# Optimization experiments

Hardware: AMD Instinct MI355X
Metric: run time of the kernel (lower is better)

The kernel has to match this reference:

```python
import jax, jax.numpy as jnp
import numpy as np

N = 100000  # num nodes


def gcn_conv(x, edge_index, W, b):
    # PyG GCNConv (eval): x' = D^-1/2 (A + I) D^-1/2 (x @ W) + b
    x = x @ W  # [N, out]
    row = jnp.concatenate([edge_index[0], jnp.arange(N)])  # sources (+ self loops)
    col = jnp.concatenate([edge_index[1], jnp.arange(N)])  # targets (+ self loops)
    ones = jnp.ones(row.shape[0], dtype=x.dtype)
    deg = jax.ops.segment_sum(ones, col, num_segments=N)
    dis = jnp.where(deg > 0, jax.lax.rsqrt(jnp.maximum(deg, 1.0)), 0.0)
    norm = dis[row] * dis[col]  # [E+N]
    msg = norm[:, None] * x[row]  # gather + scale
    out = jax.ops.segment_sum(msg, col, num_segments=N)  # scatter-add
    return out + b


def setup_inputs() -> dict:
    key = jax.random.key(0)
    k1, k2, k3, k4 = jax.random.split(key, 4)
    F_in, H, F_out = 512, 16, 40
    x = jax.random.normal(k1, (N, F_in), dtype=jnp.float32)
    edge_index = jax.random.randint(k2, (2, 3200000), 0, N, dtype=jnp.int64)
    W1 = jax.random.normal(k3, (F_in, H), dtype=jnp.float32) / np.sqrt(F_in)
    b1 = jnp.zeros((H,), dtype=jnp.float32)
    W2 = jax.random.normal(k4, (H, F_out), dtype=jnp.float32) / np.sqrt(H)
    b2 = jnp.zeros((F_out,), dtype=jnp.float32)
    return {"x": x, "edge_index": edge_index, "W1": W1, "b1": b1, "W2": W2, "b2": b2}


def reference(x, edge_index, W1, b1, W2, b2):
    # eval mode: no drop_edge, no dropout
    h = jax.nn.relu(gcn_conv(x, edge_index, W1, b1))
    return gcn_conv(h, edge_index, W2, b2)
```

## Files before the change

kernel.cpp:

```cpp
#include <hip/hip_runtime.h>

#define F_IN 512
#define HDIM 16
#define F_OUT 40
#define BTGT 64
#define REPL 8
#define NCH 512

typedef unsigned short ushortT;

__device__ __forceinline__ unsigned f2bf(float f) {
  unsigned u = __float_as_uint(f);
  u += 0x7FFF + ((u >> 16) & 1);
  return u >> 16;
}
__device__ __forceinline__ float bf2f(ushortT b) {
  return __uint_as_float(((unsigned)b) << 16);
}

__device__ __forceinline__ int load_src(const void* ei, int is64, int e) {
  return is64 ? (int)((const unsigned int*)ei)[2 * (long long)e] : ((const int*)ei)[e];
}
__device__ __forceinline__ int load_dst(const void* ei, int is64, int e, int E) {
  long long i = (long long)E + e;
  return is64 ? (int)((const unsigned int*)ei)[2 * i] : ((const int*)ei)[i];
}

extern "C" __global__ void k_init(int* __restrict__ hist, int m, int* __restrict__ flag) {
  int i = blockIdx.x * blockDim.x + threadIdx.x;
  if (i < m) hist[i] = 0;
  if (i == 0) *flag = 1;
}

extern "C" __global__ void k_detect(const unsigned int* __restrict__ w, int npairs,
                                    int* __restrict__ flag) {
  int i = blockIdx.x * blockDim.x + threadIdx.x;
  if (i < npairs && w[2 * i + 1] != 0u) atomicAnd(flag, 0);
}

extern "C" __global__ __launch_bounds__(256) void k_hist(const void* __restrict__ ei, int E,
                                                         int echunk, int* __restrict__ hist,
                                                         int NBK,
                                                         const int* __restrict__ flag) {
  extern __shared__ int lh[];
  int g = blockIdx.x, t = threadIdx.x;
  for (int i = t; i < NBK; i += 256) lh[i] = 0;
  __syncthreads();
  int is64 = *flag;
  int e0 = g * echunk;
  int e1 = e0 + echunk;
  if (e1 > E) e1 = E;
  if (e0 < e1) {
    if (is64 && ((E & 1) == 0)) {
      const int* w32 = (const int*)ei;
      int evend = e0 + ((e1 - e0) & ~1);
      for (int e = e0 + 2 * t; e + 1 < evend + 2; e += 512) {
        if (e + 1 >= e1) break;
        int4 d4 = *(const int4*)(w32 + 2 * ((size_t)E + e));
        atomicAdd(&lh[(unsigned)d4.x >> 6], 1);
        atomicAdd(&lh[(unsigned)d4.z >> 6], 1);
      }
      for (int e = evend + t; e < e1; e += 256)
        atomicAdd(&lh[(unsigned)load_dst(ei, 1, e, E) >> 6], 1);
    } else {
      for (int e = e0 + t; e < e1; e += 256)
        atomicAdd(&lh[(unsigned)load_dst(ei, is64, e, E) >> 6], 1);
    }
  }
  __syncthreads();
  int repl = g & (REPL - 1);
  for (int i = t; i < NBK; i += 256) {
    int v = lh[i];
    if (v) atomicAdd(&hist[i * REPL + repl], v);
  }
}

extern "C" __global__ __launch_bounds__(1024) void k_scanb(const int* __restrict__ hist,
                                                           int* __restrict__ boffs,
                                                           int* __restrict__ bcur, int M) {
  __shared__ int sh[1024];
  int tid = threadIdx.x;
  int C = (M + 1023) / 1024;
  int base = tid * C;
  int s = 0;
  for (int k = 0; k < C; k++) {
    int idx = base + k;
    if (idx < M) s += hist[idx];
  }
  sh[tid] = s;
  __syncthreads();
  for (int d = 1; d < 1024; d <<= 1) {
    int t2 = (tid >= d) ? sh[tid - d] : 0;
    __syncthreads();
    sh[tid] += t2;
    __syncthreads();
  }
  int run = sh[tid] - s;
  for (int k = 0; k < C; k++) {
    int idx = base + k;
    if (idx < M) {
      int v = hist[idx];
      boffs[idx] = run;
      bcur[idx] = run;
      run += v;
    }
  }
  if (tid == 1023) boffs[M] = run;
}

extern "C" __global__ __launch_bounds__(256) void k_bucket(const void* __restrict__ ei, int E,
                                                           int echunk, int* __restrict__ bcur,
                                                           unsigned int* __restrict__ bked,
                                                           const int* __restrict__ flag) {
  int g = blockIdx.x, t = threadIdx.x;
  int is64 = *flag;
  int repl = g & (REPL - 1);
  int e0 = g * echunk;
  int e1 = e0 + echunk;
  if (e1 > E) e1 = E;
  if (e0 >= e1) return;
  if (is64 && ((E & 1) == 0)) {
    const int* w32 = (const int*)ei;
    int evend = e0 + ((e1 - e0) & ~1);
    for (int e = e0 + 2 * t; e + 1 < evend + 2; e += 512) {
      if (e + 1 >= e1) break;
      int4 s4 = *(const int4*)(w32 + 2 * (size_t)e);
      int4 d4 = *(const int4*)(w32 + 2 * ((size_t)E + e));
      {
        int idx = ((unsigned)d4.x >> 6) * REPL + repl;
        int p = atomicAdd(&bcur[idx], 1);
        __builtin_nontemporal_store(
            (unsigned)s4.x | ((unsigned)(d4.x & (BTGT - 1)) << 20), &bked[p]);
      }
      {
        int idx = ((unsigned)d4.z >> 6) * REPL + repl;
        int p = atomicAdd(&bcur[idx], 1);
        __builtin_nontemporal_store(
            (unsigned)s4.z | ((unsigned)(d4.z & (BTGT - 1)) << 20), &bked[p]);
      }
    }
    for (int e = evend + t; e < e1; e += 256) {
      int r = load_src(ei, 1, e);
      int c = load_dst(ei, 1, e, E);
      int idx = ((unsigned)c >> 6) * REPL + repl;
      int p = atomicAdd(&bcur[idx], 1);
      __builtin_nontemporal_store(
          (unsigned)r | ((unsigned)(c & (BTGT - 1)) << 20), &bked[p]);
    }
  } else {
    for (int e = e0 + t; e < e1; e += 256) {
      int r = load_src(ei, is64, e);
      int c = load_dst(ei, is64, e, E);
      int idx = ((unsigned)c >> 6) * REPL + repl;
      int p = atomicAdd(&bcur[idx], 1);
      __builtin_nontemporal_store(
          (unsigned)r | ((unsigned)(c & (BTGT - 1)) << 20), &bked[p]);
    }
  }
}

extern "C" __global__ __launch_bounds__(256) void k_degb(const unsigned int* __restrict__ bked,
                                                         const int* __restrict__ boffs,
                                                         float* __restrict__ dis, int n) {
  __shared__ int lc[BTGT];
  int b = blockIdx.x, t = threadIdx.x;
  if (t < BTGT) lc[t] = 0;
  __syncthreads();
  int beg = boffs[b * REPL], end = boffs[(b + 1) * REPL];
  for (int p = beg + t; p < end; p += 256)
    atomicAdd(&lc[__builtin_nontemporal_load(&bked[p]) >> 20], 1);
  __syncthreads();
  if (t < BTGT) {
    int i = b * BTGT + t;
    if (i < n) dis[i] = rsqrtf((float)lc[t] + 1.0f);
  }
}

extern "C" __global__ __launch_bounds__(256) void k_mm1s(
    const float* __restrict__ x, const float* __restrict__ W1, const float* __restrict__ dis,
    ushortT* __restrict__ hs, int n) {
  __shared__ float xs[256 * 32];
  __shared__ float w1s[F_IN * HDIM];
  int t = threadIdx.x;
  int row0 = blockIdx.x * 256;
  {
    const float4* wg = (const float4*)W1;
    float4* wl = (float4*)w1s;
    for (int i = t; i < F_IN * HDIM / 4; i += 256) wl[i] = wg[i];
  }
  int r = row0 + t;
  bool active = (r < n);
  bool fullblk = (row0 + 255 < n);
  float acc[HDIM];
#pragma unroll
  for (int j = 0; j < HDIM; j++) acc[j] = 0.f;

  float4* xs4 = (float4*)xs;
  for (int kc = 0; kc < F_IN / 32; kc++) {
    __syncthreads();
    if (fullblk) {
#pragma unroll
      for (int it = 0; it < 8; it++) {
        int f = it * 256 + t;
        int r2 = f >> 3, fi = f & 7;
        float4 v = ((const float4*)(x + (size_t)(row0 + r2) * F_IN + kc * 32))[fi];
        xs4[r2 * 8 + (fi ^ (r2 & 7))] = v;
      }
    } else {
      for (int it = 0; it < 8; it++) {
        int f = it * 256 + t;
        int r2 = f >> 3, fi = f & 7;
        float4 v = make_float4(0.f, 0.f, 0.f, 0.f);
        if (row0 + r2 < n)
          v = ((const float4*)(x + (size_t)(row0 + r2) * F_IN + kc * 32))[fi];
        xs4[r2 * 8 + (fi ^ (r2 & 7))] = v;
      }
    }
    __syncthreads();
    if (active) {
#pragma unroll
      for (int i = 0; i < 8; i++) {
        int ii = i ^ (t & 7);
        float4 xv = xs4[t * 8 + ii];
        float xk[4] = {xv.x, xv.y, xv.z, xv.w};
        int kb = kc * 32 + i * 4;
#pragma unroll
        for (int kk = 0; kk < 4; kk++) {
          const float4* wr = (const float4*)(w1s + (size_t)(kb + kk) * HDIM);
#pragma unroll
          for (int q = 0; q < HDIM / 4; q++) {
            float4 wv = wr[q];
            acc[4 * q + 0] = fmaf(xk[kk], wv.x, acc[4 * q + 0]);
            acc[4 * q + 1] = fmaf(xk[kk], wv.y, acc[4 * q + 1]);
            acc[4 * q + 2] = fmaf(xk[kk], wv.z, acc[4 * q + 2]);
            acc[4 * q + 3] = fmaf(xk[kk], wv.w, acc[4 * q + 3]);
          }
        }
      }
    }
  }
  if (active) {
    float d = dis[r];
    unsigned wds[8];
#pragma unroll
    for (int q = 0; q < 8; q++) {
      unsigned lo = f2bf(d * acc[2 * q]);
      unsigned hi = f2bf(d * acc[2 * q + 1]);
      wds[q] = lo | (hi << 16);
    }
    uint4* o = (uint4*)(hs + (size_t)r * HDIM);
    o[0] = make_uint4(wds[0], wds[1], wds[2], wds[3]);
    o[1] = make_uint4(wds[4], wds[5], wds[6], wds[7]);
  }
}

extern "C" __global__ __launch_bounds__(256) void k_agg1(
    const ushortT* __restrict__ hs, const unsigned int* __restrict__ bked,
    const int* __restrict__ boffs, const float* __restrict__ dis,
    const float* __restrict__ b1, ushortT* __restrict__ zs, int n) {
  __shared__ float acc[BTGT * HDIM];
  int b = blockIdx.x, t = threadIdx.x;
  int g = t >> 4, j = t & 15;
  for (int k = t; k < BTGT * HDIM; k += 256) acc[k] = 0.f;
  __syncthreads();
  int beg = boffs[b * REPL], end = boffs[(b + 1) * REPL];
  int total = end - beg;
  int nfull = total >> 7;
  int pbase = beg + (g << 3);
  for (int s2 = 0; s2 < nfull; s2++) {
    int p = pbase + (s2 << 7);
    unsigned u[8];
    float v[8];
#pragma unroll
    for (int k = 0; k < 8; k++) u[k] = __builtin_nontemporal_load(&bked[p + k]);
#pragma unroll
    for (int k = 0; k < 8; k++) v[k] = bf2f(hs[(size_t)(u[k] & 0xFFFFFu) * HDIM + j]);
#pragma unroll
    for (int k = 0; k < 8; k++) atomicAdd(&acc[(u[k] >> 20) * HDIM + j], v[k]);
  }
  for (int p = beg + (nfull << 7) + g; p < end; p += 16) {
    unsigned u = __builtin_nontemporal_load(&bked[p]);
    float v = bf2f(hs[(size_t)(u & 0xFFFFFu) * HDIM + j]);
    atomicAdd(&acc[(u >> 20) * HDIM + j], v);
  }
  __syncthreads();
  for (int il = g; il < BTGT; il += 16) {
    int i = b * BTGT + il;
    if (i < n) {
      float di = dis[i];
      float v = di * (acc[il * HDIM + j] + bf2f(hs[(size_t)i * HDIM + j])) + b1[j];
      v = fmaxf(v, 0.f);
      zs[(size_t)i * HDIM + j] = (ushortT)f2bf(di * v);
    }
  }
}

extern "C" __global__ __launch_bounds__(256) void k_agg2f(
    const ushortT* __restrict__ zs, const unsigned int* __restrict__ bked,
    const int* __restrict__ boffs, const float* __restrict__ dis,
    const float* __restrict__ W2, const float* __restrict__ b2, float* __restrict__ out,
    int n) {
  __shared__ float acc[BTGT * HDIM];
  __shared__ float w2s[HDIM * F_OUT];
  __shared__ float b2s[F_OUT];
  int b = blockIdx.x, t = threadIdx.x;
  int g = t >> 4, j = t & 15;
  for (int k = t; k < BTGT * HDIM; k += 256) acc[k] = 0.f;
  for (int k = t; k < HDIM * F_OUT; k += 256) w2s[k] = W2[k];
  if (t < F_OUT) b2s[t] = b2[t];
  __syncthreads();
  int beg = boffs[b * REPL], end = boffs[(b + 1) * REPL];
  int total = end - beg;
  int nfull = total >> 7;
  int pbase = beg + (g << 3);
  for (int s2 = 0; s2 < nfull; s2++) {
    int p = pbase + (s2 << 7);
    unsigned u[8];
    float v[8];
#pragma unroll
    for (int k = 0; k < 8; k++) u[k] = __builtin_nontemporal_load(&bked[p + k]);
#pragma unroll
    for (int k = 0; k < 8; k++) v[k] = bf2f(zs[(size_t)(u[k] & 0xFFFFFu) * HDIM + j]);
#pragma unroll
    for (int k = 0; k < 8; k++) atomicAdd(&acc[(u[k] >> 20) * HDIM + j], v[k]);
  }
  for (int p = beg + (nfull << 7) + g; p < end; p += 16) {
    unsigned u = __builtin_nontemporal_load(&bked[p]);
    float v = bf2f(zs[(size_t)(u & 0xFFFFFu) * HDIM + j]);
    atomicAdd(&acc[(u >> 20) * HDIM + j], v);
  }
  __syncthreads();
  for (int il = g; il < BTGT; il += 16) {
    int i = b * BTGT + il;
    if (i < n) {
      float di = dis[i];
      acc[il * HDIM + j] = di * (acc[il * HDIM + j] + bf2f(zs[(size_t)i * HDIM + j]));
    }
  }
  __syncthreads();
  int il = t >> 2, qo = t & 3;
  int i = b * BTGT + il;
  if (i < n) {
    float tv[HDIM];
#pragma unroll
    for (int k = 0; k < HDIM; k++) tv[k] = acc[il * HDIM + k];
#pragma unroll
    for (int jj = 0; jj < 10; jj++) {
      int col = qo * 10 + jj;
      float s = b2s[col];
#pragma unroll
      for (int k = 0; k < HDIM; k++) s = fmaf(tv[k], w2s[k * F_OUT + col], s);
      out[(size_t)i * F_OUT + col] = s;
    }
  }
}

extern "C" void kernel_launch(void* const* d_in, const int* in_sizes, int n_in,
                              void* d_out, int out_size, void* d_ws, size_t ws_size,
                              hipStream_t stream) {
  const float* x = (const float*)d_in[0];
  const void* ei = d_in[1];
  const float* W1 = (const float*)d_in[2];
  const float* b1 = (const float*)d_in[3];
  const float* W2 = (const float*)d_in[4];
  const float* b2 = (const float*)d_in[5];
  float* out = (float*)d_out;

  const int n = in_sizes[0] / F_IN;
  const int E = in_sizes[1] / 2;
  const int NBK = (n + BTGT - 1) / BTGT;
  const int M = NBK * REPL;
  int echunk = (E + NCH - 1) / NCH;
  echunk = (echunk + 1) & ~1;

  char* w = (char*)d_ws;
  auto alloc = [&](size_t bytes) {
    char* p = w;
    w += (bytes + 255) & ~(size_t)255;
    return p;
  };
  int* flag = (int*)alloc(4);
  int* hist = (int*)alloc((size_t)M * 4);
  int* boffs = (int*)alloc((size_t)(M + 1) * 4);
  int* bcur = (int*)alloc((size_t)M * 4);
  float* dis = (float*)alloc((size_t)n * 4);
  unsigned int* bked = (unsigned int*)alloc((size_t)E * 4);
  ushortT* hs = (ushortT*)alloc((size_t)n * HDIM * 2);
  ushortT* zs = (ushortT*)alloc((size_t)n * HDIM * 2);

  dim3 B(256);
  hipLaunchKernelGGL(k_init, dim3((M + 255) / 256), B, 0, stream, hist, M, flag);
  int npairs = 4096;
  if (npairs > E) npairs = E;
  hipLaunchKernelGGL(k_detect, dim3((npairs + 255) / 256), B, 0, stream,
                     (const unsigned int*)ei, npairs, flag);
  hipLaunchKernelGGL(k_hist, dim3(NCH), B, (size_t)NBK * 4, stream, ei, E, echunk, hist, NBK,
                     flag);
  hipLaunchKernelGGL(k_scanb, dim3(1), dim3(1024), 0, stream, hist, boffs, bcur, M);
  hipLaunchKernelGGL(k_bucket, dim3(NCH), B, 0, stream, ei, E, echunk, bcur, bked, flag);
  hipLaunchKernelGGL(k_degb, dim3(NBK), B, 0, stream, bked, boffs, dis, n);
  hipLaunchKernelGGL(k_mm1s, dim3((n + 255) / 256), B, 0, stream, x, W1, dis, hs, n);
  hipLaunchKernelGGL(k_agg1, dim3(NBK), B, 0, stream, hs, bked, boffs, dis, b1, zs, n);
  hipLaunchKernelGGL(k_agg2f, dim3(NBK), B, 0, stream, zs, bked, boffs, dis, W2, b2, out, n);
}
```

Baseline: 962.7 us.

## Stage bucketed edges through LDS and gather two bf16 features per thread

In the degree and both aggregation kernels, each block now copies its bucketed edge list into shared memory in coalesced chunks of 2048 before processing it, replacing per-thread strided nontemporal global loads. The aggregation gather now reads a 32-bit word holding two bf16 features per thread, so 8 threads cover a 16-wide row and twice as many edges are in flight per block. Launch bounds request 2 blocks per CU. The cost is extra LDS use and two barriers per chunk, and the atomic count per thread doubles.

```diff
diff --git a/kernel.cpp b/kernel.cpp
--- a/kernel.cpp
+++ b/kernel.cpp
@@ -6,6 +6,7 @@
 #define BTGT 64
 #define REPL 8
 #define NCH 512
+#define ECH 2048
 
 typedef unsigned short ushortT;
 
@@ -16,6 +17,12 @@
 }
 __device__ __forceinline__ float bf2f(ushortT b) {
   return __uint_as_float(((unsigned)b) << 16);
+}
+__device__ __forceinline__ float bf2f_lo(unsigned w) {
+  return __uint_as_float(w << 16);
+}
+__device__ __forceinline__ float bf2f_hi(unsigned w) {
+  return __uint_as_float(w & 0xFFFF0000u);
 }
 
 __device__ __forceinline__ int load_src(const void* ei, int is64, int e) {
@@ -159,17 +166,23 @@
   }
 }
 
-extern "C" __global__ __launch_bounds__(256) void k_degb(const unsigned int* __restrict__ bked,
-                                                         const int* __restrict__ boffs,
-                                                         float* __restrict__ dis, int n) {
+extern "C" __global__ __launch_bounds__(256, 2) void k_degb(
+    const unsigned int* __restrict__ bked, const int* __restrict__ boffs,
+    float* __restrict__ dis, int n) {
   __shared__ int lc[BTGT];
+  __shared__ unsigned ebd[ECH];
   int b = blockIdx.x, t = threadIdx.x;
   if (t < BTGT) lc[t] = 0;
   __syncthreads();
   int beg = boffs[b * REPL], end = boffs[(b + 1) * REPL];
-  for (int p = beg + t; p < end; p += 256)
-    atomicAdd(&lc[__builtin_nontemporal_load(&bked[p]) >> 20], 1);
-  __syncthreads();
+  for (int cbeg = beg; cbeg < end; cbeg += ECH) {
+    int len = end - cbeg;
+    if (len > ECH) len = ECH;
+    for (int i = t; i < len; i += 256) ebd[i] = bked[cbeg + i];
+    __syncthreads();
+    for (int i = t; i < len; i += 256) atomicAdd(&lc[ebd[i] >> 20], 1);
+    __syncthreads();
+  }
   if (t < BTGT) {
     int i = b * BTGT + t;
     if (i < n) dis[i] = rsqrtf((float)lc[t] + 1.0f);
@@ -254,36 +267,56 @@
   }
 }
 
-extern "C" __global__ __launch_bounds__(256) void k_agg1(
+__device__ __forceinline__ void agg_body(const ushortT* __restrict__ feat,
+                                         const unsigned int* __restrict__ bked,
+                                         unsigned* __restrict__ eb,
+                                         float* __restrict__ acc, int beg, int end, int t) {
+  int g = t >> 3, j2 = t & 7;
+  for (int cbeg = beg; cbeg < end; cbeg += ECH) {
+    int len = end - cbeg;
+    if (len > ECH) len = ECH;
+    for (int i = t; i < len; i += 256) eb[i] = bked[cbeg + i];
+    __syncthreads();
+    int nf = len >> 8;
+    for (int s = 0; s < nf; s++) {
+      int base = (s << 8) + (g << 3);
+      unsigned u[8];
+#pragma unroll
+      for (int k = 0; k < 8; k++) u[k] = eb[base + k];
+      unsigned w[8];
+#pragma unroll
+      for (int k = 0; k < 8; k++)
+        w[k] = *(const unsigned*)(feat + ((size_t)(u[k] & 0xFFFFFu) << 4) + (j2 << 1));
+#pragma unroll
+      for (int k = 0; k < 8; k++) {
+        int a = ((u[k] >> 20) << 4) + (j2 << 1);
+        atomicAdd(&acc[a], bf2f_lo(w[k]));
+        atomicAdd(&acc[a + 1], bf2f_hi(w[k]));
+      }
+    }
+    for (int i = (nf << 8) + g; i < len; i += 32) {
+      unsigned u = eb[i];
+      unsigned w = *(const unsigned*)(feat + ((size_t)(u & 0xFFFFFu) << 4) + (j2 << 1));
+      int a = ((u >> 20) << 4) + (j2 << 1);
+      atomicAdd(&acc[a], bf2f_lo(w));
+      atomicAdd(&acc[a + 1], bf2f_hi(w));
+    }
+    __syncthreads();
+  }
+}
+
+extern "C" __global__ __launch_bounds__(256, 2) void k_agg1(
     const ushortT* __restrict__ hs, const unsigned int* __restrict__ bked,
     const int* __restrict__ boffs, const float* __restrict__ dis,
     const float* __restrict__ b1, ushortT* __restrict__ zs, int n) {
   __shared__ float acc[BTGT * HDIM];
+  __shared__ unsigned eb[ECH];
   int b = blockIdx.x, t = threadIdx.x;
+  for (int k = t; k < BTGT * HDIM; k += 256) acc[k] = 0.f;
+  __syncthreads();
+  int beg = boffs[b * REPL], end = boffs[(b + 1) * REPL];
+  agg_body(hs, bked, eb, acc, beg, end, t);
   int g = t >> 4, j = t & 15;
-  for (int k = t; k < BTGT * HDIM; k += 256) acc[k] = 0.f;
-  __syncthreads();
-  int beg = boffs[b * REPL], end = boffs[(b + 1) * REPL];
-  int total = end - beg;
-  int nfull = total >> 7;
-  int pbase = beg + (g << 3);
-  for (int s2 = 0; s2 < nfull; s2++) {
-    int p = pbase + (s2 << 7);
-    unsigned u[8];
-    float v[8];
-#pragma unroll
-    for (int k = 0; k < 8; k++) u[k] = __builtin_nontemporal_load(&bked[p + k]);
-#pragma unroll
-    for (int k = 0; k < 8; k++) v[k] = bf2f(hs[(size_t)(u[k] & 0xFFFFFu) * HDIM + j]);
-#pragma unroll
-    for (int k = 0; k < 8; k++) atomicAdd(&acc[(u[k] >> 20) * HDIM + j], v[k]);
-  }
-  for (int p = beg + (nfull << 7) + g; p < end; p += 16) {
-    unsigned u = __builtin_nontemporal_load(&bked[p]);
-    float v = bf2f(hs[(size_t)(u & 0xFFFFFu) * HDIM + j]);
-    atomicAdd(&acc[(u >> 20) * HDIM + j], v);
-  }
-  __syncthreads();
   for (int il = g; il < BTGT; il += 16) {
     int i = b * BTGT + il;
     if (i < n) {
@@ -295,41 +328,23 @@
   }
 }
 
-extern "C" __global__ __launch_bounds__(256) void k_agg2f(
+extern "C" __global__ __launch_bounds__(256, 2) void k_agg2f(
     const ushortT* __restrict__ zs, const unsigned int* __restrict__ bked,
     const int* __restrict__ boffs, const float* __restrict__ dis,
     const float* __restrict__ W2, const float* __restrict__ b2, float* __restrict__ out,
     int n) {
   __shared__ float acc[BTGT * HDIM];
+  __shared__ unsigned eb[ECH];
   __shared__ float w2s[HDIM * F_OUT];
   __shared__ float b2s[F_OUT];
   int b = blockIdx.x, t = threadIdx.x;
-  int g = t >> 4, j = t & 15;
   for (int k = t; k < BTGT * HDIM; k += 256) acc[k] = 0.f;
   for (int k = t; k < HDIM * F_OUT; k += 256) w2s[k] = W2[k];
   if (t < F_OUT) b2s[t] = b2[t];
   __syncthreads();
   int beg = boffs[b * REPL], end = boffs[(b + 1) * REPL];
-  int total = end - beg;
-  int nfull = total >> 7;
-  int pbase = beg + (g << 3);
-  for (int s2 = 0; s2 < nfull; s2++) {
-    int p = pbase + (s2 << 7);
-    unsigned u[8];
-    float v[8];
-#pragma unroll
-    for (int k = 0; k < 8; k++) u[k] = __builtin_nontemporal_load(&bked[p + k]);
-#pragma unroll
-    for (int k = 0; k < 8; k++) v[k] = bf2f(zs[(size_t)(u[k] & 0xFFFFFu) * HDIM + j]);
-#pragma unroll
-    for (int k = 0; k < 8; k++) atomicAdd(&acc[(u[k] >> 20) * HDIM + j], v[k]);
-  }
-  for (int p = beg + (nfull << 7) + g; p < end; p += 16) {
-    unsigned u = __builtin_nontemporal_load(&bked[p]);
-    float v = bf2f(zs[(size_t)(u & 0xFFFFFu) * HDIM + j]);
-    atomicAdd(&acc[(u >> 20) * HDIM + j], v);
-  }
-  __syncthreads();
+  agg_body(zs, bked, eb, acc, beg, end, t);
+  int g = t >> 4, j = t & 15;
   for (int il = g; il < BTGT; il += 16) {
     int i = b * BTGT + il;
     if (i < n) {
```

After: 969.9 us. No clear change (+0.8%).
